# Kernel tuning notes

Hardware: AMD Instinct MI355X
Metric: run time of the kernel (lower is better)

Reference implementation:

```python
import jax, jax.numpy as jnp
import numpy as np

B, L, D = 2, 2048, 1024
H = 16
HD = D // H  # 64


def _orthogonal_projection(key, d, m):
    g = jax.random.normal(key, (d, m), dtype=jnp.float32)
    q, r = jnp.linalg.qr(g)
    s = jnp.sign(jnp.diagonal(r))
    s = jnp.where(s == 0, 1.0, s)
    q = q * s[None, :]
    # preserve_variance=True
    return q * np.sqrt(d / m)


def setup_inputs() -> dict:
    key = jax.random.key(0)
    ks = jax.random.split(key, 8)
    x = jax.random.normal(ks[0], (B, L, D), dtype=jnp.float32)
    p = jax.random.normal(ks[1], (B, L, D), dtype=jnp.float32)
    s = 1.0 / np.sqrt(D)
    W_qkv = jax.random.uniform(ks[2], (3 * D, D), dtype=jnp.float32, minval=-s, maxval=s)
    b_qkv = jax.random.uniform(ks[3], (3 * D,), dtype=jnp.float32, minval=-s, maxval=s)
    W_out = jax.random.uniform(ks[4], (D, D), dtype=jnp.float32, minval=-s, maxval=s)
    b_out = jax.random.uniform(ks[5], (D,), dtype=jnp.float32, minval=-s, maxval=s)
    proj = _orthogonal_projection(ks[6], D, D // 2)
    return {"x": x, "p": p, "W_qkv": W_qkv, "b_qkv": b_qkv,
            "W_out": W_out, "b_out": b_out, "proj": proj}


def reference(x, p, W_qkv, b_qkv, W_out, b_out, proj):
    # QKV projection: (B,L,D) -> (B,L,3,H,HD)
    qkv = (jnp.einsum('bld,ed->ble', x, W_qkv) + b_qkv).reshape(B, L, 3, H, HD)
    q, k, v = qkv[:, :, 0], qkv[:, :, 1], qkv[:, :, 2]

    # Collaborative rotary phases from conditioning tokens: (B,L,H,HD/2)
    phases = (p @ proj).reshape(B, L, H, HD // 2)  # phase_scale = 1.0
    cos, sin = jnp.cos(phases), jnp.sin(phases)

    half = HD // 2
    # non-interleaved rotary: split head_dim into two halves
    def rot(t):
        t1, t2 = t[..., :half], t[..., half:]
        return jnp.concatenate([t1 * cos - t2 * sin, t1 * sin + t2 * cos], axis=-1)

    q, k = rot(q), rot(k)

    scale = HD ** -0.5
    scores = jnp.einsum('bqhd,bkhd->bhqk', q, k) * scale
    attn = jax.nn.softmax(scores, axis=-1)
    out = jnp.einsum('bhqk,bkhd->bqhd', attn, v).reshape(B, L, D)
    return jnp.einsum('bld,ed->ble', out, W_out) + b_out
```

## Files before the change

kernel.cpp:

```cpp
#include <hip/hip_runtime.h>
#include <hip/hip_bf16.h>
#include <math.h>

namespace {
constexpr int Bb = 2;
constexpr int Ll = 2048;
constexpr int Dd = 1024;
constexpr int Hh = 16;
constexpr int NT = Bb * Ll;
constexpr int D3 = 3 * Dd;
constexpr int PH = Dd / 2;
}

typedef __attribute__((ext_vector_type(8))) short bf16x8;
typedef __attribute__((ext_vector_type(4))) float f32x4;

__device__ inline unsigned pack2bf(float a, float b) {
  __hip_bfloat162 t = __float22bfloat162_rn(float2{a, b});
  union { __hip_bfloat162 h; unsigned u; } cv; cv.h = t;
  return cv.u;
}

__device__ inline float bfhalf(unsigned u, int hi) {
  union { unsigned u; float f; } c;
  c.u = hi ? (u & 0xffff0000u) : (u << 16);
  return c.f;
}

__device__ inline void async_cp16(const void* gsrc, void* ldst) {
  __builtin_amdgcn_global_load_lds(
      (const __attribute__((address_space(1))) unsigned int*)gsrc,
      (__attribute__((address_space(3))) unsigned int*)ldst, 16, 0, 0);
}

__global__ __launch_bounds__(256) void prep_kernel(
    const float4* __restrict__ p, uint2* __restrict__ p_hi4, uint2* __restrict__ p_lo4,
    const float* __restrict__ proj, short* __restrict__ th, short* __restrict__ tl,
    const float4* __restrict__ x, const float4* __restrict__ wq, const float4* __restrict__ wo,
    uint2* __restrict__ xd, uint2* __restrict__ wqd, uint2* __restrict__ wod)
{
  __shared__ float Ls[64][65];
  const int bid = blockIdx.x;
  const int tid = threadIdx.x;

  if (bid < 4096) {
    const int i = bid * 256 + tid;
    const float4 f = p[i];
    float hf[4], lf[4];
    const float ff[4] = {f.x, f.y, f.z, f.w};
#pragma unroll
    for (int j = 0; j < 4; ++j) {
      const __hip_bfloat16 h = __float2bfloat16(ff[j]);
      hf[j] = __bfloat162float(h);
      lf[j] = ff[j] - hf[j];
    }
    p_hi4[i] = make_uint2(pack2bf(hf[0], hf[1]), pack2bf(hf[2], hf[3]));
    p_lo4[i] = make_uint2(pack2bf(lf[0], lf[1]), pack2bf(lf[2], lf[3]));
  } else if (bid < 4224) {
    const int bx = bid - 4096;
    const int d0 = (bx & 15) * 64, m0 = (bx >> 4) * 64;
    const int r = tid >> 4, c4 = (tid & 15) * 4;
#pragma unroll
    for (int it = 0; it < 4; ++it) {
      const int row = it * 16 + r;
      const float4 v = *(const float4*)&proj[(size_t)(d0 + row) * PH + m0 + c4];
      Ls[row][c4] = v.x; Ls[row][c4+1] = v.y; Ls[row][c4+2] = v.z; Ls[row][c4+3] = v.w;
    }
    __syncthreads();
#pragma unroll
    for (int it = 0; it < 4; ++it) {
      const int row = it * 16 + r;
      float hf[4], lf[4];
#pragma unroll
      for (int j = 0; j < 4; ++j) {
        const float v = Ls[c4 + j][row];
        const __hip_bfloat16 h = __float2bfloat16(v);
        hf[j] = __bfloat162float(h);
        lf[j] = v - hf[j];
      }
      *(uint2*)&th[(size_t)(m0 + row) * Dd + d0 + c4] = make_uint2(pack2bf(hf[0], hf[1]), pack2bf(hf[2], hf[3]));
      *(uint2*)&tl[(size_t)(m0 + row) * Dd + d0 + c4] = make_uint2(pack2bf(lf[0], lf[1]), pack2bf(lf[2], lf[3]));
    }
  } else {
    int i = (bid - 4224) * 256 + tid;
    const float4* s; uint2* d;
    if (i < 1048576) { s = x; d = xd; }
    else if (i < 1048576 + 786432) { i -= 1048576; s = wq; d = wqd; }
    else { i -= 1048576 + 786432; s = wo; d = wod; }
    const float4 f = s[i];
    d[i] = make_uint2(pack2bf(f.x, f.y), pack2bf(f.z, f.w));
  }
}

__global__ __launch_bounds__(256) void gemm_nn_split(
    const short* __restrict__ Ah_g, const short* __restrict__ Al_g,
    const short* __restrict__ Wh_g, const short* __restrict__ Wl_g,
    float* __restrict__ C)
{
  __shared__ __align__(16) short Ah[2][64 * 32], Al[2][64 * 32];
  __shared__ __align__(16) short Wh[2][64 * 32], Wl[2][64 * 32];
  const int tid = threadIdx.x;
  const int w = tid >> 6, lane = tid & 63;
  const int l15 = lane & 15, quad = lane >> 4;
  const int n0 = blockIdx.y * 64, m0 = blockIdx.x * 64;

  const int row = tid >> 2, cc = tid & 3;
  const int ksw = (cc ^ (row & 3)) * 8;
  const short* gAh = Ah_g + (size_t)(n0 + row) * Dd + ksw;
  const short* gAl = Al_g + (size_t)(n0 + row) * Dd + ksw;
  const short* gWh = Wh_g + (size_t)(m0 + row) * Dd + ksw;
  const short* gWl = Wl_g + (size_t)(m0 + row) * Dd + ksw;

  f32x4 acc[4];
#pragma unroll
  for (int j = 0; j < 4; ++j) acc[j] = f32x4{0.f, 0.f, 0.f, 0.f};

  const int swq = (quad ^ (l15 & 3)) * 8;

#define STAGE_NN(kv, bf) { \
  async_cp16(gAh + (kv), &Ah[bf][tid * 8]); \
  async_cp16(gAl + (kv), &Al[bf][tid * 8]); \
  async_cp16(gWh + (kv), &Wh[bf][tid * 8]); \
  async_cp16(gWl + (kv), &Wl[bf][tid * 8]); }

  STAGE_NN(0, 0);
  int cur = 0;
  for (int k0 = 0; k0 < Dd; k0 += 32) {
    __syncthreads();
    if (k0 + 32 < Dd) STAGE_NN(k0 + 32, cur ^ 1);

    bf16x8 ah, al, wh[4], wl[4];
    ah = *(const bf16x8*)&Ah[cur][(w * 16 + l15) * 32 + swq];
    al = *(const bf16x8*)&Al[cur][(w * 16 + l15) * 32 + swq];
#pragma unroll
    for (int j = 0; j < 4; ++j) {
      wh[j] = *(const bf16x8*)&Wh[cur][(j * 16 + l15) * 32 + swq];
      wl[j] = *(const bf16x8*)&Wl[cur][(j * 16 + l15) * 32 + swq];
    }
#pragma unroll
    for (int j = 0; j < 4; ++j) {
      acc[j] = __builtin_amdgcn_mfma_f32_16x16x32_bf16(ah, wh[j], acc[j], 0, 0, 0);
      acc[j] = __builtin_amdgcn_mfma_f32_16x16x32_bf16(ah, wl[j], acc[j], 0, 0, 0);
      acc[j] = __builtin_amdgcn_mfma_f32_16x16x32_bf16(al, wh[j], acc[j], 0, 0, 0);
    }
    cur ^= 1;
  }
#undef STAGE_NN

#pragma unroll
  for (int r = 0; r < 4; ++r) {
    float* crow = C + (size_t)(n0 + w * 16 + quad * 4 + r) * PH + m0 + l15;
#pragma unroll
    for (int j = 0; j < 4; ++j) crow[j * 16] = acc[j][r];
  }
}

__global__ __launch_bounds__(256) void gemm_qkv_fused(
    const __hip_bfloat16* __restrict__ A, const __hip_bfloat16* __restrict__ W,
    const float* __restrict__ bias, const float* __restrict__ phases,
    __hip_bfloat16* __restrict__ q_bf, __hip_bfloat16* __restrict__ k_bf,
    __hip_bfloat16* __restrict__ vt_g)
{
  __shared__ __align__(16) short As[2][128 * 32];
  __shared__ __align__(16) short Ws[2][128 * 32];
  const int tid = threadIdx.x;
  const int w = tid >> 6, lane = tid & 63;
  const int l15 = lane & 15, quad = lane >> 4;
  const int wn = w >> 1, wm = w & 1;
  const int n0 = blockIdx.y * 128, m0 = blockIdx.x * 128;

  const int row = tid >> 2, cc = tid & 3;
  const int ksw = (cc ^ (row & 3)) * 8;
  const short* gA  = (const short*)A + (size_t)(n0 + row) * Dd + ksw;
  const short* gW  = (const short*)W + (size_t)(m0 + row) * Dd + ksw;

  f32x4 acc[4][4];
#pragma unroll
  for (int i = 0; i < 4; ++i)
#pragma unroll
    for (int j = 0; j < 4; ++j) acc[i][j] = f32x4{0.f, 0.f, 0.f, 0.f};

  const int swq = (quad ^ (l15 & 3)) * 8;

#define STAGE_QKV(kv, bf) { \
  async_cp16(gA + (kv),            &As[bf][tid * 8]); \
  async_cp16(gA + 64 * Dd + (kv),  &As[bf][2048 + tid * 8]); \
  async_cp16(gW + (kv),            &Ws[bf][tid * 8]); \
  async_cp16(gW + 64 * Dd + (kv),  &Ws[bf][2048 + tid * 8]); }

  STAGE_QKV(0, 0);
  int cur = 0;
  for (int k0 = 0; k0 < Dd; k0 += 32) {
    __syncthreads();
    if (k0 + 32 < Dd) STAGE_QKV(k0 + 32, cur ^ 1);

    bf16x8 af[4], bf[4];
#pragma unroll
    for (int i = 0; i < 4; ++i)
      af[i] = *(const bf16x8*)&As[cur][(wn * 64 + i * 16 + l15) * 32 + swq];
#pragma unroll
    for (int j = 0; j < 4; ++j)
      bf[j] = *(const bf16x8*)&Ws[cur][(wm * 64 + j * 16 + l15) * 32 + swq];
#pragma unroll
    for (int i = 0; i < 4; ++i)
#pragma unroll
      for (int j = 0; j < 4; ++j)
        acc[i][j] = __builtin_amdgcn_mfma_f32_16x16x32_bf16(af[i], bf[j], acc[i][j], 0, 0, 0);
    cur ^= 1;
  }
#undef STAGE_QKV

  float bv[4];
#pragma unroll
  for (int j = 0; j < 4; ++j) bv[j] = bias[m0 + wm * 64 + j * 16 + l15];

  const int region = m0 >> 10;
  const int mloc = (m0 & 1023) + wm * 64;
  const int h = mloc >> 6;

  if (region < 2) {
    __hip_bfloat16* dst = region == 0 ? q_bf : k_bf;
    const float SC = region == 0 ? 0.18033688011112042f : 1.0f;
    const int dosw = (region == 1);
#pragma unroll
    for (int i = 0; i < 4; ++i)
#pragma unroll
      for (int r = 0; r < 4; ++r) {
        const int n = n0 + wn * 64 + i * 16 + quad * 4 + r;
        const int swz = dosw ? (((quad * 4 + r) & 7) << 3) : 0;
        const float* phrow = phases + (size_t)n * PH + h * 32;
        __hip_bfloat16* drow = dst + (size_t)n * Dd + h * 64;
#pragma unroll
        for (int pz = 0; pz < 2; ++pz) {
          const float ph = phrow[pz * 16 + l15];
          float sn, cs;
          __sincosf(ph, &sn, &cs);
          const float a1 = acc[i][pz][r] + bv[pz];
          const float a2 = acc[i][pz + 2][r] + bv[pz + 2];
          drow[(pz * 16 + l15) ^ swz]      = __float2bfloat16((a1 * cs - a2 * sn) * SC);
          drow[(pz * 16 + 32 + l15) ^ swz] = __float2bfloat16((a1 * sn + a2 * cs) * SC);
        }
      }
  } else {
    const int bh = (n0 >> 11) * 16 + h;
    const int tokb = (n0 & 2047) + wn * 64;
    const int vsw = (l15 & 7) << 3;
#pragma unroll
    for (int i = 0; i < 4; ++i)
#pragma unroll
      for (int j = 0; j < 4; ++j) {
        const uint2 o = make_uint2(
            pack2bf(acc[i][j][0] + bv[j], acc[i][j][1] + bv[j]),
            pack2bf(acc[i][j][2] + bv[j], acc[i][j][3] + bv[j]));
        const int d = j * 16 + l15;
        *(uint2*)&vt_g[(size_t)(bh * 64 + d) * Ll + tokb + ((i * 16 + quad * 4) ^ vsw)] = o;
      }
  }
}

__global__ __launch_bounds__(256) void gemm_bt_64(
    const __hip_bfloat16* __restrict__ A, const __hip_bfloat16* __restrict__ W,
    const float* __restrict__ bias, float* __restrict__ C, int K, int M)
{
  __shared__ __align__(16) short As[2][128 * 32];
  __shared__ __align__(16) short Ws[2][64 * 32];
  const int tid = threadIdx.x;
  const int w = tid >> 6, lane = tid & 63;
  const int l15 = lane & 15, quad = lane >> 4;
  const int n0 = blockIdx.y * 128, m0 = blockIdx.x * 64;

  const int row = tid >> 2, cc = tid & 3;
  const int ksw = (cc ^ (row & 3)) * 8;
  const short* gA = (const short*)A + (size_t)(n0 + row) * K + ksw;
  const short* gW = (const short*)W + (size_t)(m0 + row) * K + ksw;

  f32x4 acc[2][4];
#pragma unroll
  for (int i = 0; i < 2; ++i)
#pragma unroll
    for (int j = 0; j < 4; ++j) acc[i][j] = f32x4{0.f, 0.f, 0.f, 0.f};

  const int swq = (quad ^ (l15 & 3)) * 8;

#define STAGE_BT(kv, bf) { \
  async_cp16(gA + (kv),           &As[bf][tid * 8]); \
  async_cp16(gA + 64 * K + (kv),  &As[bf][2048 + tid * 8]); \
  async_cp16(gW + (kv),           &Ws[bf][tid * 8]); }

  STAGE_BT(0, 0);
  int cur = 0;
  for (int k0 = 0; k0 < K; k0 += 32) {
    __syncthreads();
    if (k0 + 32 < K) STAGE_BT(k0 + 32, cur ^ 1);

    bf16x8 af[2], bf[4];
#pragma unroll
    for (int i = 0; i < 2; ++i)
      af[i] = *(const bf16x8*)&As[cur][(w * 32 + i * 16 + l15) * 32 + swq];
#pragma unroll
    for (int j = 0; j < 4; ++j)
      bf[j] = *(const bf16x8*)&Ws[cur][(j * 16 + l15) * 32 + swq];
#pragma unroll
    for (int i = 0; i < 2; ++i)
#pragma unroll
      for (int j = 0; j < 4; ++j)
        acc[i][j] = __builtin_amdgcn_mfma_f32_16x16x32_bf16(af[i], bf[j], acc[i][j], 0, 0, 0);
    cur ^= 1;
  }
#undef STAGE_BT

  float bv[4];
#pragma unroll
  for (int j = 0; j < 4; ++j) bv[j] = bias[m0 + j * 16 + l15];
#pragma unroll
  for (int i = 0; i < 2; ++i)
#pragma unroll
    for (int r = 0; r < 4; ++r) {
      float* crow = C + (size_t)(n0 + w * 32 + i * 16 + quad * 4 + r) * M + m0 + l15;
#pragma unroll
      for (int j = 0; j < 4; ++j) crow[j * 16] = acc[i][j][r] + bv[j];
    }
}

__global__ __launch_bounds__(256) void attn_mfma(
    const __hip_bfloat16* __restrict__ q_bf,
    const __hip_bfloat16* __restrict__ k_bf,
    const __hip_bfloat16* __restrict__ vt_g,
    __hip_bfloat16* __restrict__ o_part,
    float* __restrict__ lden_g)
{
  __shared__ __align__(16) short Kb[2][4096];
  __shared__ __align__(16) short Vb[2][4096];

  const int tid = threadIdx.x;
  const int w = tid >> 6;
  const int lane = tid & 63;
  const int l15 = lane & 15;
  const int quad = lane >> 4;

  const int q0 = blockIdx.x * 128;
  const int bh = blockIdx.y;
  const int kz = blockIdx.z;
  const int b = bh >> 4, h = bh & 15;
  const int kt0 = kz * 16;

  bf16x8 qfrag[2][2];
#pragma unroll
  for (int qg = 0; qg < 2; ++qg)
#pragma unroll
    for (int kh = 0; kh < 2; ++kh) {
      const size_t qrow = (size_t)(b * Ll + q0 + w * 32 + qg * 16 + l15);
      qfrag[qg][kh] = *(const bf16x8*)(q_bf + qrow * Dd + h * 64 + kh * 32 + quad * 8);
    }

  f32x4 acc[4][2];
#pragma unroll
  for (int dt = 0; dt < 4; ++dt)
#pragma unroll
    for (int qg = 0; qg < 2; ++qg) acc[dt][qg] = f32x4{0.f, 0.f, 0.f, 0.f};
  f32x4 lden[2] = {f32x4{0.f,0.f,0.f,0.f}, f32x4{0.f,0.f,0.f,0.f}};
  const f32x4 zro = {0.f, 0.f, 0.f, 0.f};
  const short one_bf = (short)0x3F80;
  const bf16x8 ones8 = {one_bf, one_bf, one_bf, one_bf, one_bf, one_bf, one_bf, one_bf};

  const __hip_bfloat16* ksrc = k_bf + ((size_t)(b * Ll) + (tid >> 3)) * Dd + h * 64 + (tid & 7) * 8;
  const __hip_bfloat16* vsrc = vt_g + ((size_t)(bh * 64) + (tid >> 3)) * Ll + (tid & 7) * 8;
  const int ldst = tid * 8;

  const int sw = (l15 & 7) << 3;
  const int co0 = (quad * 8) ^ sw;
  const int co1 = (32 + quad * 8) ^ sw;

#define STAGE_K(t, bf) { const __hip_bfloat16* kp_ = ksrc + (size_t)(t) * 64 * Dd; \
  async_cp16(kp_, &Kb[bf][ldst]); async_cp16(kp_ + (size_t)32 * Dd, &Kb[bf][2048 + ldst]); }
#define STAGE_V(t, bf) { const __hip_bfloat16* vp_ = vsrc + (size_t)(t) * 64; \
  async_cp16(vp_, &Vb[bf][ldst]); async_cp16(vp_ + (size_t)32 * Ll, &Vb[bf][2048 + ldst]); }

  f32x4 s[4][2];

#define QK_N(Ks, n) { \
  const bf16x8 af0_ = *(const bf16x8*)&(Ks)[((n) * 16 + l15) * 64 + co0]; \
  const bf16x8 af1_ = *(const bf16x8*)&(Ks)[((n) * 16 + l15) * 64 + co1]; \
  s[n][0] = __builtin_amdgcn_mfma_f32_16x16x32_bf16(af0_, qfrag[0][0], zro, 0, 0, 0); \
  s[n][1] = __builtin_amdgcn_mfma_f32_16x16x32_bf16(af0_, qfrag[1][0], zro, 0, 0, 0); \
  s[n][0] = __builtin_amdgcn_mfma_f32_16x16x32_bf16(af1_, qfrag[0][1], s[n][0], 0, 0, 0); \
  s[n][1] = __builtin_amdgcn_mfma_f32_16x16x32_bf16(af1_, qfrag[1][1], s[n][1], 0, 0, 0); }

#define EXPPACK(v, dst) { union { float f; unsigned u; } p0_, p1_, p2_, p3_; \
  p0_.f = __builtin_amdgcn_exp2f((v)[0]); p1_.f = __builtin_amdgcn_exp2f((v)[1]); \
  p2_.f = __builtin_amdgcn_exp2f((v)[2]); p3_.f = __builtin_amdgcn_exp2f((v)[3]); \
  dst = make_uint2(__builtin_amdgcn_perm(p1_.u, p0_.u, 0x07060302u), \
                   __builtin_amdgcn_perm(p3_.u, p2_.u, 0x07060302u)); }

#define PV_QG(va, aU, cU, qg) { \
  auto rx32_ = __builtin_amdgcn_permlane32_swap((aU).x, (cU).x, false, false); \
  auto rx16_ = __builtin_amdgcn_permlane16_swap(rx32_[0], rx32_[1], false, false); \
  auto ry32_ = __builtin_amdgcn_permlane32_swap((aU).y, (cU).y, false, false); \
  auto ry16_ = __builtin_amdgcn_permlane16_swap(ry32_[0], ry32_[1], false, false); \
  union { unsigned u[4]; bf16x8 v; } pb_; \
  pb_.u[0] = rx16_[0]; pb_.u[1] = ry16_[0]; pb_.u[2] = rx16_[1]; pb_.u[3] = ry16_[1]; \
  lden[qg] = __builtin_amdgcn_mfma_f32_16x16x32_bf16(ones8, pb_.v, lden[qg], 0, 0, 0); \
  acc[0][qg] = __builtin_amdgcn_mfma_f32_16x16x32_bf16(va[0], pb_.v, acc[0][qg], 0, 0, 0); \
  acc[1][qg] = __builtin_amdgcn_mfma_f32_16x16x32_bf16(va[1], pb_.v, acc[1][qg], 0, 0, 0); \
  acc[2][qg] = __builtin_amdgcn_mfma_f32_16x16x32_bf16(va[2], pb_.v, acc[2][qg], 0, 0, 0); \
  acc[3][qg] = __builtin_amdgcn_mfma_f32_16x16x32_bf16(va[3], pb_.v, acc[3][qg], 0, 0, 0); }

  STAGE_K(kt0, 0);
  __syncthreads();
  STAGE_K(kt0 + 1, 1);
  STAGE_V(kt0, 0);
  __builtin_amdgcn_s_setprio(1);
  QK_N(Kb[0], 0); QK_N(Kb[0], 1); QK_N(Kb[0], 2); QK_N(Kb[0], 3);
  __builtin_amdgcn_s_setprio(0);

  for (int i = 0; i < 16; ++i) {
    __syncthreads();
    if (i + 2 < 16) STAGE_K(kt0 + i + 2, i & 1);
    if (i + 1 < 16) STAGE_V(kt0 + i + 1, (i + 1) & 1);
    const short* Kn = &Kb[(i + 1) & 1][0];
    const short* Vc = &Vb[i & 1][0];
    const bool doqk = (i + 1 < 16);

    uint2 a0, a1, c0, c1;
    EXPPACK(s[0][0], a0); EXPPACK(s[0][1], a1);
    EXPPACK(s[1][0], c0); EXPPACK(s[1][1], c1);
    if (doqk) {
      __builtin_amdgcn_s_setprio(1);
      QK_N(Kn, 0); QK_N(Kn, 1);
      __builtin_amdgcn_s_setprio(0);
    }
    {
      bf16x8 va[4];
#pragma unroll
      for (int dt = 0; dt < 4; ++dt)
        va[dt] = *(const bf16x8*)&Vc[(dt * 16 + l15) * 64 + co0];
      __builtin_amdgcn_s_setprio(1);
      PV_QG(va, a0, c0, 0);
      PV_QG(va, a1, c1, 1);
      __builtin_amdgcn_s_setprio(0);
    }

    uint2 a2, a3, c2, c3;
    EXPPACK(s[2][0], a2); EXPPACK(s[2][1], a3);
    EXPPACK(s[3][0], c2); EXPPACK(s[3][1], c3);
    if (doqk) {
      __builtin_amdgcn_s_setprio(1);
      QK_N(Kn, 2); QK_N(Kn, 3);
      __builtin_amdgcn_s_setprio(0);
    }
    {
      bf16x8 va[4];
#pragma unroll
      for (int dt = 0; dt < 4; ++dt)
        va[dt] = *(const bf16x8*)&Vc[(dt * 16 + l15) * 64 + co1];
      __builtin_amdgcn_s_setprio(1);
      PV_QG(va, a2, c2, 0);
      PV_QG(va, a3, c3, 1);
      __builtin_amdgcn_s_setprio(0);
    }
  }

#undef STAGE_K
#undef STAGE_V
#undef QK_N
#undef EXPPACK
#undef PV_QG

#pragma unroll
  for (int qg = 0; qg < 2; ++qg) {
    const float lv = lden[qg][0];
    const float linv = 1.f / lv;
    const int ql = q0 + w * 32 + qg * 16 + l15;
    if (quad == 0)
      lden_g[((size_t)(kz * Bb + b) * Hh + h) * Ll + ql] = lv;
    __hip_bfloat16* dst = o_part + ((size_t)kz * NT + b * Ll + ql) * Dd + h * 64;
#pragma unroll
    for (int dt = 0; dt < 4; ++dt) {
      const uint2 o = make_uint2(
          pack2bf(acc[dt][qg][0] * linv, acc[dt][qg][1] * linv),
          pack2bf(acc[dt][qg][2] * linv, acc[dt][qg][3] * linv));
      *(uint2*)&dst[dt * 16 + quad * 4] = o;
    }
  }
}

__global__ __launch_bounds__(256) void attn_combine(
    const __hip_bfloat16* __restrict__ o_part, const float* __restrict__ lden_g,
    __hip_bfloat16* __restrict__ aout)
{
  const int i = blockIdx.x * 256 + threadIdx.x;
  const int n = i >> 8, d4 = i & 255;
  const int b = n >> 11, l = n & 2047;
  const int h = d4 >> 4;
  const float l0 = lden_g[((size_t)b * Hh + h) * Ll + l];
  const float l1 = lden_g[((size_t)(Bb + b) * Hh + h) * Ll + l];
  const float inv = 1.f / (l0 + l1);
  const float w0 = l0 * inv, w1 = l1 * inv;
  const uint2 a0 = ((const uint2*)o_part)[i];
  const uint2 a1 = ((const uint2*)o_part)[(NT * (size_t)Dd / 4) + i];
  const float r0 = w0 * bfhalf(a0.x, 0) + w1 * bfhalf(a1.x, 0);
  const float r1 = w0 * bfhalf(a0.x, 1) + w1 * bfhalf(a1.x, 1);
  const float r2 = w0 * bfhalf(a0.y, 0) + w1 * bfhalf(a1.y, 0);
  const float r3 = w0 * bfhalf(a0.y, 1) + w1 * bfhalf(a1.y, 1);
  ((uint2*)aout)[i] = make_uint2(pack2bf(r0, r1), pack2bf(r2, r3));
}

extern "C" void kernel_launch(void* const* d_in, const int* in_sizes, int n_in,
                              void* d_out, int out_size, void* d_ws, size_t ws_size,
                              hipStream_t stream) {
  const float* x     = (const float*)d_in[0];
  const float* p     = (const float*)d_in[1];
  const float* W_qkv = (const float*)d_in[2];
  const float* b_qkv = (const float*)d_in[3];
  const float* W_out = (const float*)d_in[4];
  const float* b_out = (const float*)d_in[5];
  const float* proj  = (const float*)d_in[6];
  float* out = (float*)d_out;

  char* wsb = (char*)d_ws;
  float*          phases   = (float*)(wsb);
  short*          p_hi     = (short*)(wsb + (8u << 20));
  __hip_bfloat16* aout_bf  = (__hip_bfloat16*)(wsb + (8u << 20));
  short*          p_lo     = (short*)(wsb + (16u << 20));
  __hip_bfloat16* vt_g     = (__hip_bfloat16*)(wsb + (16u << 20));
  short*          projt_hi = (short*)(wsb + (24u << 20));
  short*          projt_lo = (short*)(wsb + (25u << 20));
  __hip_bfloat16* q_bf     = (__hip_bfloat16*)(wsb + (26u << 20));
  __hip_bfloat16* k_bf     = (__hip_bfloat16*)(wsb + (34u << 20));
  __hip_bfloat16* x_bf     = (__hip_bfloat16*)(wsb + (42u << 20));
  __hip_bfloat16* o_part   = (__hip_bfloat16*)(wsb + (42u << 20));
  __hip_bfloat16* wqkv_bf  = (__hip_bfloat16*)(wsb + (50u << 20));
  __hip_bfloat16* wout_bf  = (__hip_bfloat16*)(wsb + (58u << 20));
  float*          lden_g   = (float*)(wsb + (60u << 20));

  prep_kernel<<<12416, 256, 0, stream>>>(
      (const float4*)p, (uint2*)p_hi, (uint2*)p_lo,
      proj, projt_hi, projt_lo,
      (const float4*)x, (const float4*)W_qkv, (const float4*)W_out,
      (uint2*)x_bf, (uint2*)wqkv_bf, (uint2*)wout_bf);
  gemm_nn_split<<<dim3(PH / 64, NT / 64), 256, 0, stream>>>(p_hi, p_lo, projt_hi, projt_lo, phases);
  gemm_qkv_fused<<<dim3(D3 / 128, NT / 128), 256, 0, stream>>>(x_bf, wqkv_bf, b_qkv, phases,
                                                               q_bf, k_bf, vt_g);
  attn_mfma<<<dim3(Ll / 128, Bb * Hh, 2), 256, 0, stream>>>(q_bf, k_bf, vt_g, o_part, lden_g);
  attn_combine<<<4096, 256, 0, stream>>>(o_part, lden_g, aout_bf);
  gemm_bt_64<<<dim3(Dd / 64, NT / 128), 256, 0, stream>>>(aout_bf, wout_bf, b_out, out, Dd, Dd);
}
```

Before: 266.4 us.

## Triple-buffer GEMM shared-memory staging with explicit vmcnt waits

Moves the three GEMM kernels (phase projection, QKV, output projection) from double to triple buffering in LDS, prefetching two k-tiles ahead. The old __syncthreads is replaced by partial s_waitcnt vmcnt plus a raw s_barrier, so loads for later tiles can stay in flight while the current tile is computed. The goal is to hide global-load latency behind MFMA work. In exchange it uses more LDS, which may lower occupancy, and correctness depends on the hand-counted vmcnt values matching the number of async copies per stage.

```diff
diff --git a/kernel.cpp b/kernel.cpp
--- a/kernel.cpp
+++ b/kernel.cpp
@@ -97,8 +97,8 @@
     const short* __restrict__ Wh_g, const short* __restrict__ Wl_g,
     float* __restrict__ C)
 {
-  __shared__ __align__(16) short Ah[2][64 * 32], Al[2][64 * 32];
-  __shared__ __align__(16) short Wh[2][64 * 32], Wl[2][64 * 32];
+  __shared__ __align__(16) short Ah[3][64 * 32], Al[3][64 * 32];
+  __shared__ __align__(16) short Wh[3][64 * 32], Wl[3][64 * 32];
   const int tid = threadIdx.x;
   const int w = tid >> 6, lane = tid & 63;
   const int l15 = lane & 15, quad = lane >> 4;
@@ -124,18 +124,22 @@
   async_cp16(gWl + (kv), &Wl[bf][tid * 8]); }
 
   STAGE_NN(0, 0);
-  int cur = 0;
+  STAGE_NN(32, 1);
+  int bi = 0;
   for (int k0 = 0; k0 < Dd; k0 += 32) {
-    __syncthreads();
-    if (k0 + 32 < Dd) STAGE_NN(k0 + 32, cur ^ 1);
+    if (k0 + 32 < Dd) { asm volatile("s_waitcnt vmcnt(4)" ::: "memory"); }
+    else              { asm volatile("s_waitcnt vmcnt(0)" ::: "memory"); }
+    __builtin_amdgcn_s_barrier();
+    __builtin_amdgcn_sched_barrier(0);
+    if (k0 + 64 < Dd) { const int bn = (bi + 2 >= 3) ? bi - 1 : bi + 2; STAGE_NN(k0 + 64, bn); }
 
     bf16x8 ah, al, wh[4], wl[4];
-    ah = *(const bf16x8*)&Ah[cur][(w * 16 + l15) * 32 + swq];
-    al = *(const bf16x8*)&Al[cur][(w * 16 + l15) * 32 + swq];
+    ah = *(const bf16x8*)&Ah[bi][(w * 16 + l15) * 32 + swq];
+    al = *(const bf16x8*)&Al[bi][(w * 16 + l15) * 32 + swq];
 #pragma unroll
     for (int j = 0; j < 4; ++j) {
-      wh[j] = *(const bf16x8*)&Wh[cur][(j * 16 + l15) * 32 + swq];
-      wl[j] = *(const bf16x8*)&Wl[cur][(j * 16 + l15) * 32 + swq];
+      wh[j] = *(const bf16x8*)&Wh[bi][(j * 16 + l15) * 32 + swq];
+      wl[j] = *(const bf16x8*)&Wl[bi][(j * 16 + l15) * 32 + swq];
     }
 #pragma unroll
     for (int j = 0; j < 4; ++j) {
@@ -143,7 +147,7 @@
       acc[j] = __builtin_amdgcn_mfma_f32_16x16x32_bf16(ah, wl[j], acc[j], 0, 0, 0);
       acc[j] = __builtin_amdgcn_mfma_f32_16x16x32_bf16(al, wh[j], acc[j], 0, 0, 0);
     }
-    cur ^= 1;
+    bi = (bi == 2) ? 0 : bi + 1;
   }
 #undef STAGE_NN
 
@@ -161,8 +165,8 @@
     __hip_bfloat16* __restrict__ q_bf, __hip_bfloat16* __restrict__ k_bf,
     __hip_bfloat16* __restrict__ vt_g)
 {
-  __shared__ __align__(16) short As[2][128 * 32];
-  __shared__ __align__(16) short Ws[2][128 * 32];
+  __shared__ __align__(16) short As[3][128 * 32];
+  __shared__ __align__(16) short Ws[3][128 * 32];
   const int tid = threadIdx.x;
   const int w = tid >> 6, lane = tid & 63;
   const int l15 = lane & 15, quad = lane >> 4;
@@ -189,24 +193,28 @@
   async_cp16(gW + 64 * Dd + (kv),  &Ws[bf][2048 + tid * 8]); }
 
   STAGE_QKV(0, 0);
-  int cur = 0;
+  STAGE_QKV(32, 1);
+  int bi = 0;
   for (int k0 = 0; k0 < Dd; k0 += 32) {
-    __syncthreads();
-    if (k0 + 32 < Dd) STAGE_QKV(k0 + 32, cur ^ 1);
+    if (k0 + 32 < Dd) { asm volatile("s_waitcnt vmcnt(4)" ::: "memory"); }
+    else              { asm volatile("s_waitcnt vmcnt(0)" ::: "memory"); }
+    __builtin_amdgcn_s_barrier();
+    __builtin_amdgcn_sched_barrier(0);
+    if (k0 + 64 < Dd) { const int bn = (bi + 2 >= 3) ? bi - 1 : bi + 2; STAGE_QKV(k0 + 64, bn); }
 
     bf16x8 af[4], bf[4];
 #pragma unroll
     for (int i = 0; i < 4; ++i)
-      af[i] = *(const bf16x8*)&As[cur][(wn * 64 + i * 16 + l15) * 32 + swq];
+      af[i] = *(const bf16x8*)&As[bi][(wn * 64 + i * 16 + l15) * 32 + swq];
 #pragma unroll
     for (int j = 0; j < 4; ++j)
-      bf[j] = *(const bf16x8*)&Ws[cur][(wm * 64 + j * 16 + l15) * 32 + swq];
+      bf[j] = *(const bf16x8*)&Ws[bi][(wm * 64 + j * 16 + l15) * 32 + swq];
 #pragma unroll
     for (int i = 0; i < 4; ++i)
 #pragma unroll
       for (int j = 0; j < 4; ++j)
         acc[i][j] = __builtin_amdgcn_mfma_f32_16x16x32_bf16(af[i], bf[j], acc[i][j], 0, 0, 0);
-    cur ^= 1;
+    bi = (bi == 2) ? 0 : bi + 1;
   }
 #undef STAGE_QKV
 
@@ -262,8 +270,8 @@
     const __hip_bfloat16* __restrict__ A, const __hip_bfloat16* __restrict__ W,
     const float* __restrict__ bias, float* __restrict__ C, int K, int M)
 {
-  __shared__ __align__(16) short As[2][128 * 32];
-  __shared__ __align__(16) short Ws[2][64 * 32];
+  __shared__ __align__(16) short As[3][128 * 32];
+  __shared__ __align__(16) short Ws[3][64 * 32];
   const int tid = threadIdx.x;
   const int w = tid >> 6, lane = tid & 63;
   const int l15 = lane & 15, quad = lane >> 4;
@@ -288,24 +296,28 @@
   async_cp16(gW + (kv),           &Ws[bf][tid * 8]); }
 
   STAGE_BT(0, 0);
-  int cur = 0;
+  STAGE_BT(32, 1);
+  int bi = 0;
   for (int k0 = 0; k0 < K; k0 += 32) {
-    __syncthreads();
-    if (k0 + 32 < K) STAGE_BT(k0 + 32, cur ^ 1);
+    if (k0 + 32 < K) { asm volatile("s_waitcnt vmcnt(3)" ::: "memory"); }
+    else             { asm volatile("s_waitcnt vmcnt(0)" ::: "memory"); }
+    __builtin_amdgcn_s_barrier();
+    __builtin_amdgcn_sched_barrier(0);
+    if (k0 + 64 < K) { const int bn = (bi + 2 >= 3) ? bi - 1 : bi + 2; STAGE_BT(k0 + 64, bn); }
 
     bf16x8 af[2], bf[4];
 #pragma unroll
     for (int i = 0; i < 2; ++i)
-      af[i] = *(const bf16x8*)&As[cur][(w * 32 + i * 16 + l15) * 32 + swq];
+      af[i] = *(const bf16x8*)&As[bi][(w * 32 + i * 16 + l15) * 32 + swq];
 #pragma unroll
     for (int j = 0; j < 4; ++j)
-      bf[j] = *(const bf16x8*)&Ws[cur][(j * 16 + l15) * 32 + swq];
+      bf[j] = *(const bf16x8*)&Ws[bi][(j * 16 + l15) * 32 + swq];
 #pragma unroll
     for (int i = 0; i < 2; ++i)
 #pragma unroll
       for (int j = 0; j < 4; ++j)
         acc[i][j] = __builtin_amdgcn_mfma_f32_16x16x32_bf16(af[i], bf[j], acc[i][j], 0, 0, 0);
-    cur ^= 1;
+    bi = (bi == 2) ? 0 : bi + 1;
   }
 #undef STAGE_BT
 
```

New measurement: 252.8 us, median of 2. -5.1%, faster.
